# Optimization experiments

Hardware: AMD Instinct MI355X
Metric: run time of the kernel (lower is better)

Reference implementation:

```python
import jax, jax.numpy as jnp
import numpy as np

WS = 4        # window size
NH = 8        # num heads
GN_GROUPS = 8 # min(8, hidden_dim)
EPS = 1e-5


def group_norm(x, gamma, beta, groups=GN_GROUPS, eps=EPS):
    # x: [B, C, H, W]
    B, C, H, W = x.shape
    xr = x.reshape(B, groups, C // groups, H, W)
    mu = xr.mean(axis=(2, 3, 4), keepdims=True)
    var = xr.var(axis=(2, 3, 4), keepdims=True)
    xn = ((xr - mu) / jnp.sqrt(var + eps)).reshape(B, C, H, W)
    return xn * gamma[None, :, None, None] + beta[None, :, None, None]


def setup_inputs() -> dict:
    key = jax.random.key(0)
    ks = jax.random.split(key, 8)
    B, Cin, Ch, H, W = 4, 64, 256, 128, 128
    sc = 0.02
    return {
        "x": jax.random.normal(ks[0], (B, Cin, H, W), dtype=jnp.float32),
        "h": jax.random.normal(ks[1], (B, Ch, H, W), dtype=jnp.float32),
        "c": jax.random.normal(ks[2], (B, Ch, H, W), dtype=jnp.float32),
        "in_proj_w": jax.random.normal(ks[3], (Ch, Cin + Ch), dtype=jnp.float32) * sc,
        "in_proj_b": jnp.zeros((Ch,), jnp.float32),
        "ln_g": jnp.ones((Ch,), jnp.float32),
        "ln_b": jnp.zeros((Ch,), jnp.float32),
        "qkv_w": jax.random.normal(ks[4], (3 * Ch, Ch), dtype=jnp.float32) * sc,
        "qkv_b": jnp.zeros((3 * Ch,), jnp.float32),
        "proj_w": jax.random.normal(ks[5], (Ch, Ch), dtype=jnp.float32) * sc,
        "proj_b": jnp.zeros((Ch,), jnp.float32),
        "gates_w": jax.random.normal(ks[6], (4 * Ch, Ch), dtype=jnp.float32) * sc,
        "gates_b": jnp.zeros((4 * Ch,), jnp.float32),
        "gn_g": jnp.ones((Ch,), jnp.float32),
        "gn_b": jnp.zeros((Ch,), jnp.float32),
    }


def reference(x, h, c, in_proj_w, in_proj_b, ln_g, ln_b, qkv_w, qkv_b,
              proj_w, proj_b, gates_w, gates_b, gn_g, gn_b):
    B, Cin, H, W = x.shape
    Ch = h.shape[1]
    ws, nh = WS, NH
    hd = Ch // nh
    nHw, nWw = H // ws, W // ws  # H,W divisible by ws -> no padding branch

    # in_proj: 1x1 conv on concat([x, h])
    comb = jnp.concatenate([x, h], axis=1)  # [B, Cin+Ch, H, W]
    p = jnp.einsum('bchw,oc->bohw', comb, in_proj_w) + in_proj_b[None, :, None, None]

    # window partition -> [B*nWin, ws*ws, Ch]
    xw = p.reshape(B, Ch, nHw, ws, nWw, ws)
    xw = xw.transpose(0, 2, 4, 3, 5, 1).reshape(B * nHw * nWw, ws * ws, Ch)

    # pre-attention LayerNorm
    mu = xw.mean(-1, keepdims=True)
    var = xw.var(-1, keepdims=True)
    xn = (xw - mu) / jnp.sqrt(var + EPS) * ln_g + ln_b

    # multi-head attention within each 16-token window
    Bw, N, _ = xn.shape
    qkv = (xn @ qkv_w.T + qkv_b).reshape(Bw, N, 3, nh, hd)
    q, k, v = qkv[:, :, 0], qkv[:, :, 1], qkv[:, :, 2]  # [Bw, N, nh, hd]
    attn = jnp.einsum('bqhd,bkhd->bhqk', q, k) * (hd ** -0.5)
    attn = jax.nn.softmax(attn, axis=-1)
    out = jnp.einsum('bhqk,bkhd->bqhd', attn, v).reshape(Bw, N, Ch)
    out = out @ proj_w.T + proj_b

    # window unpartition -> [B, Ch, H, W]
    am = out.reshape(B, nHw, nWw, ws, ws, Ch)
    am = am.transpose(0, 5, 1, 3, 2, 4).reshape(B, Ch, H, W)

    am = group_norm(am, gn_g, gn_b)  # eval mode: dropout2d is identity

    # LSTM gates via 1x1 conv
    gates = jnp.einsum('bchw,oc->bohw', am, gates_w) + gates_b[None, :, None, None]
    ci, cf, co, cg = jnp.split(gates, 4, axis=1)
    i = jax.nn.sigmoid(ci)
    f = jax.nn.sigmoid(cf)
    o = jax.nn.sigmoid(co)
    g = jnp.tanh(cg)
    cnext = f * c + i * g
    hnext = group_norm(o * jnp.tanh(cnext), gn_g, gn_b)
    return hnext, cnext
```

## Files before the change

### kernel.cpp

```cpp
#include <hip/hip_runtime.h>

#define DI __device__ __forceinline__

typedef unsigned short ushort_t;
typedef __attribute__((ext_vector_type(8))) short bf16x8;
typedef __attribute__((ext_vector_type(4))) float f32x4;
typedef __attribute__((ext_vector_type(4))) unsigned short us4;
typedef __attribute__((ext_vector_type(8))) unsigned short us8;

constexpr float EPSF = 1e-5f;

constexpr size_t O_WIP  = 0;
constexpr size_t O_WQKV = 163840;
constexpr size_t O_WPRJ = 557056;
constexpr size_t O_WGAT = 688128;
constexpr size_t O_MU   = 1212416;
constexpr size_t O_RSTD = 1474560;
constexpr size_t O_GN   = 1736704;
constexpr size_t O_FIN  = 1737216;
constexpr size_t O_R2   = 1740800;
constexpr size_t O_R3   = O_R2 + 33554432;
constexpr size_t O_R1   = O_R3 + 33554432;

DI ushort_t f2b(float f) {
  unsigned u = __float_as_uint(f);
  u += 0x7fff + ((u >> 16) & 1);
  return (ushort_t)(u >> 16);
}
DI float b2f(ushort_t s) { return __uint_as_float(((unsigned)s) << 16); }

DI void cp16(ushort_t* lds, const ushort_t* g) {
  __builtin_amdgcn_global_load_lds(
      (const __attribute__((address_space(1))) unsigned*)g,
      (__attribute__((address_space(3))) unsigned*)lds, 16, 0, 0);
}

__global__ __launch_bounds__(256) void k_prep(const float* __restrict__ ipw,
    const float* __restrict__ qkvw, const float* __restrict__ projw,
    const float* __restrict__ gatesw, ushort_t* __restrict__ d0,
    ushort_t* __restrict__ d1, ushort_t* __restrict__ d2, ushort_t* __restrict__ d3) {
  int i = blockIdx.x * 256 + threadIdx.x;
  if (i < 81920)  { d0[i] = f2b(ipw[i]);    return; }
  i -= 81920;
  if (i < 196608) { d1[i] = f2b(qkvw[i]);   return; }
  i -= 196608;
  if (i < 65536)  { d2[i] = f2b(projw[i]);  return; }
  i -= 65536;
  if (i < 262144) { d3[i] = f2b(gatesw[i]); return; }
}

__global__ __launch_bounds__(256) void k_comb(const float* __restrict__ x,
    const float* __restrict__ h, ushort_t* __restrict__ comb) {
  __shared__ float tile[32][257];
  const int tid = threadIdx.x;
  const int wid = blockIdx.x;
  const int b = wid / 640, r = wid % 640, ct = r / 64, pt = r % 64;
  const int p0 = pt * 256;
#pragma unroll 8
  for (int i = 0; i < 32; ++i) {
    const int cg = ct * 32 + i;
    const float* src = (cg < 64) ? x + (((size_t)(b * 64 + cg)) << 14)
                                 : h + (((size_t)(b * 256 + (cg - 64))) << 14);
    tile[i][tid] = src[p0 + tid];
  }
  __syncthreads();
  const int c = tid & 31;
#pragma unroll 8
  for (int i2 = 0; i2 < 32; ++i2) {
    const int tl = (tid >> 5) + i2 * 8;
    comb[(size_t)((b << 14) + p0 + tl) * 320 + ct * 32 + c] = f2b(tile[c][tl]);
  }
}

template<int K, int KT, bool GATESB>
DI void gemm_main(const ushort_t* __restrict__ A, const ushort_t* __restrict__ B,
                  int t0, int nb, ushort_t* smem, f32x4 acc[4][4]) {
  const int tid = threadIdx.x;
  const int lane = tid & 63, wave = tid >> 6;
  const int w2 = wave * 2;
  const int wm = wave >> 1, wn = wave & 1;
  const int kfs = lane >> 4, cc = lane & 15;
  const int aoff = kfs * 1024 + (wm * 64 + cc) * 8;
  const int boff = 4096 + kfs * 1024 + (wn * 64 + cc) * 8;

  auto stage = [&](int buf, int k0) {
#pragma unroll
    for (int i = 0; i < 2; ++i) {
      const int w2i = w2 + i;
      const int kslot = w2i >> 1;
      const int mrow = ((w2i & 1) << 6) + lane;
      const ushort_t* ga = A + (size_t)(t0 + mrow) * K + k0 + kslot * 8;
      cp16(smem + buf * 8192 + w2i * 512, ga);
      int ng;
      if (GATESB) ng = ((mrow >> 5) << 8) + nb + (mrow & 31);
      else        ng = nb + mrow;
      const ushort_t* gb = B + (size_t)ng * K + k0 + kslot * 8;
      cp16(smem + buf * 8192 + 4096 + w2i * 512, gb);
    }
  };

  stage(0, 0);
  __syncthreads();
  for (int kt = 0; kt < KT; ++kt) {
    const int cur = (kt & 1) * 8192;
    if (kt + 1 < KT) stage((kt & 1) ^ 1, (kt + 1) * 32);
    bf16x8 a0 = *(const bf16x8*)(smem + cur + aoff);
    bf16x8 a1 = *(const bf16x8*)(smem + cur + aoff + 128);
    bf16x8 a2 = *(const bf16x8*)(smem + cur + aoff + 256);
    bf16x8 a3 = *(const bf16x8*)(smem + cur + aoff + 384);
    bf16x8 b0 = *(const bf16x8*)(smem + cur + boff);
    bf16x8 b1 = *(const bf16x8*)(smem + cur + boff + 128);
    bf16x8 b2 = *(const bf16x8*)(smem + cur + boff + 256);
    bf16x8 b3 = *(const bf16x8*)(smem + cur + boff + 384);
    acc[0][0] = __builtin_amdgcn_mfma_f32_16x16x32_bf16(a0, b0, acc[0][0], 0, 0, 0);
    acc[0][1] = __builtin_amdgcn_mfma_f32_16x16x32_bf16(a0, b1, acc[0][1], 0, 0, 0);
    acc[0][2] = __builtin_amdgcn_mfma_f32_16x16x32_bf16(a0, b2, acc[0][2], 0, 0, 0);
    acc[0][3] = __builtin_amdgcn_mfma_f32_16x16x32_bf16(a0, b3, acc[0][3], 0, 0, 0);
    acc[1][0] = __builtin_amdgcn_mfma_f32_16x16x32_bf16(a1, b0, acc[1][0], 0, 0, 0);
    acc[1][1] = __builtin_amdgcn_mfma_f32_16x16x32_bf16(a1, b1, acc[1][1], 0, 0, 0);
    acc[1][2] = __builtin_amdgcn_mfma_f32_16x16x32_bf16(a1, b2, acc[1][2], 0, 0, 0);
    acc[1][3] = __builtin_amdgcn_mfma_f32_16x16x32_bf16(a1, b3, acc[1][3], 0, 0, 0);
    acc[2][0] = __builtin_amdgcn_mfma_f32_16x16x32_bf16(a2, b0, acc[2][0], 0, 0, 0);
    acc[2][1] = __builtin_amdgcn_mfma_f32_16x16x32_bf16(a2, b1, acc[2][1], 0, 0, 0);
    acc[2][2] = __builtin_amdgcn_mfma_f32_16x16x32_bf16(a2, b2, acc[2][2], 0, 0, 0);
    acc[2][3] = __builtin_amdgcn_mfma_f32_16x16x32_bf16(a2, b3, acc[2][3], 0, 0, 0);
    acc[3][0] = __builtin_amdgcn_mfma_f32_16x16x32_bf16(a3, b0, acc[3][0], 0, 0, 0);
    acc[3][1] = __builtin_amdgcn_mfma_f32_16x16x32_bf16(a3, b1, acc[3][1], 0, 0, 0);
    acc[3][2] = __builtin_amdgcn_mfma_f32_16x16x32_bf16(a3, b2, acc[3][2], 0, 0, 0);
    acc[3][3] = __builtin_amdgcn_mfma_f32_16x16x32_bf16(a3, b3, acc[3][3], 0, 0, 0);
    __syncthreads();
  }
}

template<int NTOT>
DI void epi_store(f32x4 acc[4][4], ushort_t* __restrict__ C, const float* __restrict__ bias,
                  int t0, int n0g) {
  const int tid = threadIdx.x, lane = tid & 63, wave = tid >> 6;
  const int wm = wave >> 1, wn = wave & 1;
  const int r0 = (lane >> 4) * 4, cc = lane & 15;
#pragma unroll
  for (int fn = 0; fn < 4; ++fn) {
    const int n = wn * 64 + fn * 16 + cc;
    const float bv = bias[n0g + n];
#pragma unroll
    for (int fm = 0; fm < 4; ++fm) {
#pragma unroll
      for (int r = 0; r < 4; ++r) {
        const int m = wm * 64 + fm * 16 + r0 + r;
        C[(size_t)(t0 + m) * NTOT + n0g + n] = f2b(acc[fm][fn][r] + bv);
      }
    }
  }
}

__global__ __launch_bounds__(256) void k_inproj(const ushort_t* __restrict__ A,
    const ushort_t* __restrict__ B, const float* __restrict__ bias, ushort_t* __restrict__ C) {
  __shared__ ushort_t smem[16384];
  const int wid = blockIdx.x, g = wid & 7, s = wid >> 3;
  const int mt = g * 64 + s / 2, nt = s % 2;
  f32x4 acc[4][4] = {};
  gemm_main<320, 10, false>(A, B, mt * 128, nt * 128, smem, acc);
  epi_store<256>(acc, C, bias, mt * 128, nt * 128);
}

__global__ __launch_bounds__(256) void k_qkv(const ushort_t* __restrict__ A,
    const ushort_t* __restrict__ B, const float* __restrict__ bias, ushort_t* __restrict__ C) {
  __shared__ ushort_t smem[16384];
  const int wid = blockIdx.x, g = wid & 7, s = wid >> 3;
  const int mt = g * 64 + s / 6, nt = s % 6;
  f32x4 acc[4][4] = {};
  gemm_main<256, 8, false>(A, B, mt * 128, nt * 128, smem, acc);
  epi_store<768>(acc, C, bias, mt * 128, nt * 128);
}

__global__ __launch_bounds__(256) void k_proj(const ushort_t* __restrict__ A,
    const ushort_t* __restrict__ B, const float* __restrict__ bias, ushort_t* __restrict__ C,
    float* __restrict__ gnsum) {
  __shared__ ushort_t smem[16384];
  const int wid = blockIdx.x, g = wid & 7, s = wid >> 3;
  const int mt = g * 64 + s / 2, nt = s % 2;
  const int t0 = mt * 128, n0g = nt * 128;
  f32x4 acc[4][4] = {};
  gemm_main<256, 8, false>(A, B, t0, n0g, smem, acc);
  const int tid = threadIdx.x, lane = tid & 63, wave = tid >> 6;
  const int wm = wave >> 1, wn = wave & 1;
  const int r0 = (lane >> 4) * 4, cc = lane & 15;
  float sA = 0.f, s2A = 0.f, sB = 0.f, s2B = 0.f;
#pragma unroll
  for (int fn = 0; fn < 4; ++fn) {
    const int n = wn * 64 + fn * 16 + cc;
    const float bv = bias[n0g + n];
#pragma unroll
    for (int fm = 0; fm < 4; ++fm) {
#pragma unroll
      for (int r = 0; r < 4; ++r) {
        const int m = wm * 64 + fm * 16 + r0 + r;
        const float v = acc[fm][fn][r] + bv;
        C[(size_t)(t0 + m) * 256 + n0g + n] = f2b(v);
        if (fn < 2) { sA += v; s2A += v * v; } else { sB += v; s2B += v * v; }
      }
    }
  }
#pragma unroll
  for (int o = 32; o; o >>= 1) {
    sA += __shfl_down(sA, o); s2A += __shfl_down(s2A, o);
    sB += __shfl_down(sB, o); s2B += __shfl_down(s2B, o);
  }
  if (lane == 0) {
    const int bch = t0 >> 14;
    const int gb0 = (n0g >> 5) + wn * 2;
    atomicAdd(&gnsum[bch * 8 + gb0], sA);      atomicAdd(&gnsum[32 + bch * 8 + gb0], s2A);
    atomicAdd(&gnsum[bch * 8 + gb0 + 1], sB);  atomicAdd(&gnsum[32 + bch * 8 + gb0 + 1], s2B);
  }
}

__global__ __launch_bounds__(256) void k_gates(const ushort_t* __restrict__ A,
    const ushort_t* __restrict__ B, const float* __restrict__ gbias,
    const float* __restrict__ cin, float* __restrict__ cnext, float* __restrict__ u,
    float* __restrict__ gnsum2) {
  __shared__ ushort_t smem[16512];
  const int wid = blockIdx.x, g = wid & 7, s = wid >> 3;
  const int mt = g * 64 + (s >> 3), nt = s & 7;
  const int t0 = mt * 128, ch0 = nt * 32;
  f32x4 acc[4][4] = {};
  gemm_main<256, 8, true>(A, B, t0, ch0, smem, acc);

  float* cs = (float*)smem;
  const int tid = threadIdx.x, lane = tid & 63, wave = tid >> 6;
  const int wm = wave >> 1, wn = wave & 1;
  const int r0 = (lane >> 4) * 4, cc = lane & 15;
  const int bch = t0 >> 14, pix0 = t0 & 16383;
  const int cl = tid >> 3, tq = tid & 7;
  const int ch = ch0 + cl;
  const float bi = gbias[ch], bf_ = gbias[256 + ch];
  const float bo = gbias[512 + ch], bg = gbias[768 + ch];
  float ssum = 0.f, ssq = 0.f;
#pragma unroll
  for (int mh = 0; mh < 2; ++mh) {
    __syncthreads();
    if (wm == mh) {
#pragma unroll
      for (int fm = 0; fm < 4; ++fm)
#pragma unroll
        for (int fn = 0; fn < 4; ++fn)
#pragma unroll
          for (int r = 0; r < 4; ++r)
            cs[(fm * 16 + r0 + r) * 129 + wn * 64 + fn * 16 + cc] = acc[fm][fn][r];
    }
    __syncthreads();
    const size_t base = (((size_t)(bch * 256 + ch)) << 14) + pix0 + mh * 64 + tq * 8;
    float cv[8], cn[8], uv[8];
    *(float4*)cv       = *(const float4*)(cin + base);
    *(float4*)(cv + 4) = *(const float4*)(cin + base + 4);
#pragma unroll
    for (int i = 0; i < 8; ++i) {
      const int t = tq * 8 + i;
      const float zi = cs[t * 129 + cl] + bi;
      const float zf = cs[t * 129 + 32 + cl] + bf_;
      const float zo = cs[t * 129 + 64 + cl] + bo;
      const float zg = cs[t * 129 + 96 + cl] + bg;
      const float iv = 1.f / (1.f + expf(-zi));
      const float fv = 1.f / (1.f + expf(-zf));
      const float ov = 1.f / (1.f + expf(-zo));
      const float gv = tanhf(zg);
      const float c2 = fv * cv[i] + iv * gv;
      cn[i] = c2;
      const float uu = ov * tanhf(c2);
      uv[i] = uu; ssum += uu; ssq += uu * uu;
    }
    *(float4*)(cnext + base)     = *(float4*)cn;
    *(float4*)(cnext + base + 4) = *(float4*)(cn + 4);
    *(float4*)(u + base)         = *(float4*)uv;
    *(float4*)(u + base + 4)     = *(float4*)(uv + 4);
  }
#pragma unroll
  for (int o = 32; o; o >>= 1) { ssum += __shfl_down(ssum, o); ssq += __shfl_down(ssq, o); }
  if (lane == 0) {
    atomicAdd(&gnsum2[bch * 8 + nt], ssum);
    atomicAdd(&gnsum2[32 + bch * 8 + nt], ssq);
  }
}

__global__ __launch_bounds__(256) void k_lnstats(const ushort_t* __restrict__ p,
    float* __restrict__ mu, float* __restrict__ rstd) {
  const int wave = threadIdx.x >> 6, lane = threadIdx.x & 63;
  const int t = blockIdx.x * 4 + wave;
  us4 v = *(const us4*)(p + (size_t)t * 256 + lane * 4);
  const float a = b2f(v[0]), b = b2f(v[1]), c = b2f(v[2]), d = b2f(v[3]);
  float s = a + b + c + d, s2 = a * a + b * b + c * c + d * d;
#pragma unroll
  for (int o = 32; o; o >>= 1) { s += __shfl_down(s, o); s2 += __shfl_down(s2, o); }
  if (lane == 0) {
    const float m = s * (1.f / 256.f);
    const float var = s2 * (1.f / 256.f) - m * m;
    mu[t] = m;
    rstd[t] = rsqrtf(fmaxf(var, 0.f) + EPSF);
  }
}

__global__ __launch_bounds__(256) void k_xn(const ushort_t* __restrict__ p,
    const float* __restrict__ mu, const float* __restrict__ rstd,
    const float* __restrict__ lg, const float* __restrict__ lb, ushort_t* __restrict__ xn) {
  const size_t i = ((size_t)blockIdx.x * 256 + threadIdx.x) * 8;
  const int t = (int)(i >> 8), c = (int)(i & 255);
  const float m = mu[t], r = rstd[t];
  us8 v = *(const us8*)(p + i);
  us8 o;
#pragma unroll
  for (int e = 0; e < 8; ++e)
    o[e] = f2b((b2f(v[e]) - m) * r * lg[c + e] + lb[c + e]);
  *(us8*)(xn + i) = o;
}

__global__ __launch_bounds__(128) void k_attn(const ushort_t* __restrict__ qkvb,
    ushort_t* __restrict__ ao) {
  __shared__ float ks[4224], vs[4224];
  const int tid = threadIdx.x;
  const int wid = blockIdx.x;
  const int b = wid >> 10, rem = wid & 1023, wh = rem >> 5, wc = rem & 31;
  const int tbase = (b << 14) + wh * 512 + wc * 4;
#pragma unroll 4
  for (int it = 0; it < 16; ++it) {
    const int i = it * 128 + tid;
    const int j = i >> 7, q = i & 127;
    const int which = q >> 6, hh2 = (q >> 3) & 7, d4 = (q & 7) << 2;
    const int tj = tbase + ((j >> 2) << 7) + (j & 3);
    us4 v = *(const us4*)(qkvb + (size_t)tj * 768 + 256 + which * 256 + hh2 * 32 + d4);
    float* dst = (which ? vs : ks) + (hh2 * 16 + j) * 33 + d4;
    dst[0] = b2f(v[0]); dst[1] = b2f(v[1]); dst[2] = b2f(v[2]); dst[3] = b2f(v[3]);
  }
  const int hh = tid >> 4, qi = tid & 15;
  const int tq = tbase + ((qi >> 2) << 7) + (qi & 3);
  float qv[32];
  {
    const ushort_t* qp = qkvb + (size_t)tq * 768 + hh * 32;
#pragma unroll
    for (int uq = 0; uq < 8; ++uq) {
      us4 v = *(const us4*)(qp + uq * 4);
#pragma unroll
      for (int e = 0; e < 4; ++e) qv[uq * 4 + e] = b2f(v[e]);
    }
  }
  __syncthreads();
  float sc[16];
#pragma unroll
  for (int j = 0; j < 16; ++j) {
    const float* kr = ks + (hh * 16 + j) * 33;
    float s = 0.f;
#pragma unroll
    for (int u2 = 0; u2 < 32; ++u2) s = fmaf(qv[u2], kr[u2], s);
    sc[j] = s * 0.17677669529663687f;
  }
  float m = sc[0];
#pragma unroll
  for (int j = 1; j < 16; ++j) m = fmaxf(m, sc[j]);
  float ssum = 0.f;
#pragma unroll
  for (int j = 0; j < 16; ++j) { sc[j] = __expf(sc[j] - m); ssum += sc[j]; }
  const float inv = 1.f / ssum;
  float oacc[32] = {};
#pragma unroll
  for (int j = 0; j < 16; ++j) {
    const float p = sc[j] * inv;
    const float* vr = vs + (hh * 16 + j) * 33;
#pragma unroll
    for (int u2 = 0; u2 < 32; ++u2) oacc[u2] = fmaf(p, vr[u2], oacc[u2]);
  }
  unsigned* dst = (unsigned*)(ao + (size_t)tq * 256 + hh * 32);
#pragma unroll
  for (int uq = 0; uq < 16; ++uq)
    dst[uq] = (unsigned)f2b(oacc[2 * uq]) | ((unsigned)f2b(oacc[2 * uq + 1]) << 16);
}

__global__ void k_gnfin(const float* __restrict__ sums, float* __restrict__ fin) {
  const int i = threadIdx.x;
  const float invN = 1.f / 524288.f;
  const float m = sums[i] * invN;
  const float var = sums[32 + i] * invN - m * m;
  fin[i] = m;
  fin[32 + i] = rsqrtf(fmaxf(var, 0.f) + EPSF);
}

__global__ __launch_bounds__(256) void k_amn(const ushort_t* __restrict__ am,
    const float* __restrict__ fin, const float* __restrict__ gg,
    const float* __restrict__ gb, ushort_t* __restrict__ amn) {
  const size_t i = ((size_t)blockIdx.x * 256 + threadIdx.x) * 8;
  const int t = (int)(i >> 8), c = (int)(i & 255);
  const int b = t >> 14, grp = c >> 5;
  const float m = fin[b * 8 + grp], r = fin[32 + b * 8 + grp];
  us8 v = *(const us8*)(am + i);
  us8 o;
#pragma unroll
  for (int e = 0; e < 8; ++e)
    o[e] = f2b((b2f(v[e]) - m) * r * gg[c + e] + gb[c + e]);
  *(us8*)(amn + i) = o;
}

__global__ __launch_bounds__(256) void k_gnapply(const float* __restrict__ u,
    const float* __restrict__ fin2, const float* __restrict__ gg,
    const float* __restrict__ gb, float* __restrict__ hout) {
  const size_t base = ((size_t)blockIdx.x * 256 + threadIdx.x) * 4;
  const int b = (int)(base >> 22);
  const int ch = (int)((base >> 14) & 255);
  const int grp = ch >> 5;
  const float m = fin2[b * 8 + grp], r = fin2[32 + b * 8 + grp];
  const float gv = gg[ch], bv = gb[ch];
  float4 v = *(const float4*)(u + base);
  v.x = (v.x - m) * r * gv + bv;
  v.y = (v.y - m) * r * gv + bv;
  v.z = (v.z - m) * r * gv + bv;
  v.w = (v.w - m) * r * gv + bv;
  *(float4*)(hout + base) = v;
}

extern "C" void kernel_launch(void* const* d_in, const int* in_sizes, int n_in,
                              void* d_out, int out_size, void* d_ws, size_t ws_size,
                              hipStream_t stream) {
  const float* x      = (const float*)d_in[0];
  const float* h      = (const float*)d_in[1];
  const float* c      = (const float*)d_in[2];
  const float* ipw    = (const float*)d_in[3];
  const float* ipb    = (const float*)d_in[4];
  const float* lng    = (const float*)d_in[5];
  const float* lnb    = (const float*)d_in[6];
  const float* qkvw   = (const float*)d_in[7];
  const float* qkvb   = (const float*)d_in[8];
  const float* projw  = (const float*)d_in[9];
  const float* projb  = (const float*)d_in[10];
  const float* gatesw = (const float*)d_in[11];
  const float* gatesb = (const float*)d_in[12];
  const float* gng    = (const float*)d_in[13];
  const float* gnb    = (const float*)d_in[14];
  char* wsb  = (char*)d_ws;
  float* out = (float*)d_out;

  ushort_t* wip  = (ushort_t*)(wsb + O_WIP);
  ushort_t* wqkv = (ushort_t*)(wsb + O_WQKV);
  ushort_t* wprj = (ushort_t*)(wsb + O_WPRJ);
  ushort_t* wgat = (ushort_t*)(wsb + O_WGAT);
  float* mu_a    = (float*)(wsb + O_MU);
  float* rstd_a  = (float*)(wsb + O_RSTD);
  float* gnsum   = (float*)(wsb + O_GN);
  float* gnfin   = (float*)(wsb + O_FIN);
  ushort_t* R2   = (ushort_t*)(wsb + O_R2);
  ushort_t* R3   = (ushort_t*)(wsb + O_R3);
  ushort_t* R1   = (ushort_t*)(wsb + O_R1);

  hipMemsetAsync(gnsum, 0, 512, stream);
  k_prep<<<2368, 256, 0, stream>>>(ipw, qkvw, projw, gatesw, wip, wqkv, wprj, wgat);
  k_comb<<<2560, 256, 0, stream>>>(x, h, R1);
  k_inproj<<<1024, 256, 0, stream>>>(R1, wip, ipb, R2);
  k_lnstats<<<16384, 256, 0, stream>>>(R2, mu_a, rstd_a);
  k_xn<<<8192, 256, 0, stream>>>(R2, mu_a, rstd_a, lng, lnb, R3);
  k_qkv<<<3072, 256, 0, stream>>>(R3, wqkv, qkvb, R1);
  k_attn<<<4096, 128, 0, stream>>>(R1, R2);
  k_proj<<<1024, 256, 0, stream>>>(R2, wprj, projb, R3, gnsum);
  k_gnfin<<<1, 32, 0, stream>>>(gnsum, gnfin);
  k_amn<<<8192, 256, 0, stream>>>(R3, gnfin, gng, gnb, R2);
  k_gates<<<4096, 256, 0, stream>>>(R2, wgat, gatesb, c, out + 16777216, (float*)R1,
                                    gnsum + 64);
  k_gnfin<<<1, 32, 0, stream>>>(gnsum + 64, gnfin + 64);
  k_gnapply<<<16384, 256, 0, stream>>>((float*)R1, gnfin + 64, gng, gnb, out);
}
```

Before: 821.1 us.

## Fuse LayerNorm into in_proj GEMM and compute LSTM gates in registers

Replaces the in_proj GEMM plus separate LN-stats and normalize kernels with one kernel that uses 64-token by 256-channel tiles, so each block holds full rows and can compute LayerNorm in its epilogue. This drops two launches and one round trip of the bf16 intermediate through global memory. The gates kernel reorders which weight rows it loads, so each wave's accumulators hold the i/f/o/g gates for the same channels. The epilogue therefore works straight from registers with no LDS transpose and no syncs, using fast exp-based sigmoid/tanh at some accuracy cost. The new in_proj tile has less per-block reuse of A, and the gates kernel now does 4-wide stores instead of 8-wide.

```diff
diff --git a/kernel.cpp b/kernel.cpp
--- a/kernel.cpp
+++ b/kernel.cpp
@@ -14,8 +14,6 @@
 constexpr size_t O_WQKV = 163840;
 constexpr size_t O_WPRJ = 557056;
 constexpr size_t O_WGAT = 688128;
-constexpr size_t O_MU   = 1212416;
-constexpr size_t O_RSTD = 1474560;
 constexpr size_t O_GN   = 1736704;
 constexpr size_t O_FIN  = 1737216;
 constexpr size_t O_R2   = 1740800;
@@ -28,6 +26,13 @@
   return (ushort_t)(u >> 16);
 }
 DI float b2f(ushort_t s) { return __uint_as_float(((unsigned)s) << 16); }
+
+DI float fsig(float x) { return 1.f / (1.f + __expf(-x)); }
+DI float ftanh(float x) {
+  const float e = __expf(-2.f * fabsf(x));
+  const float t = (1.f - e) / (1.f + e);
+  return copysignf(t, x);
+}
 
 DI void cp16(ushort_t* lds, const ushort_t* g) {
   __builtin_amdgcn_global_load_lds(
@@ -92,7 +97,7 @@
       const ushort_t* ga = A + (size_t)(t0 + mrow) * K + k0 + kslot * 8;
       cp16(smem + buf * 8192 + w2i * 512, ga);
       int ng;
-      if (GATESB) ng = ((mrow >> 5) << 8) + nb + (mrow & 31);
+      if (GATESB) ng = ((mrow >> 4) & 3) * 256 + nb + ((mrow >> 6) << 4) + (mrow & 15);
       else        ng = nb + mrow;
       const ushort_t* gb = B + (size_t)ng * K + k0 + kslot * 8;
       cp16(smem + buf * 8192 + 4096 + w2i * 512, gb);
@@ -153,14 +158,97 @@
   }
 }
 
-__global__ __launch_bounds__(256) void k_inproj(const ushort_t* __restrict__ A,
-    const ushort_t* __restrict__ B, const float* __restrict__ bias, ushort_t* __restrict__ C) {
-  __shared__ ushort_t smem[16384];
-  const int wid = blockIdx.x, g = wid & 7, s = wid >> 3;
-  const int mt = g * 64 + s / 2, nt = s % 2;
+__global__ __launch_bounds__(256) void k_inproj_ln(const ushort_t* __restrict__ A,
+    const ushort_t* __restrict__ B, const float* __restrict__ bias,
+    const float* __restrict__ lg, const float* __restrict__ lb, ushort_t* __restrict__ xn) {
+  __shared__ ushort_t smem[20480];
+  __shared__ float red[4][2][64];
+  __shared__ float fin[2][64];
+  const int tid = threadIdx.x, lane = tid & 63, wave = tid >> 6;
+  const int t0 = blockIdx.x * 64;
+  const int kfs = lane >> 4, cc = lane & 15;
+  const int r0 = kfs * 4;
+  const int aoff = kfs * 512 + cc * 8;
+  const int boff = 2048 + kfs * 2048 + (wave * 64 + cc) * 8;
+
+  auto stage = [&](int buf, int k0) {
+#pragma unroll
+    for (int rr = 0; rr < 5; ++rr) {
+      const int r = wave * 5 + rr;
+      const int e = r * 64 + lane;
+      const ushort_t* src;
+      if (r < 4) src = A + (size_t)(t0 + (e & 63)) * 320 + k0 + (e >> 6) * 8;
+      else { const int e2 = e - 256; src = B + (size_t)(e2 & 255) * 320 + k0 + (e2 >> 8) * 8; }
+      cp16(smem + buf * 10240 + r * 512, src);
+    }
+  };
+
+  stage(0, 0);
   f32x4 acc[4][4] = {};
-  gemm_main<320, 10, false>(A, B, mt * 128, nt * 128, smem, acc);
-  epi_store<256>(acc, C, bias, mt * 128, nt * 128);
+  __syncthreads();
+  for (int kt = 0; kt < 10; ++kt) {
+    const int cur = (kt & 1) * 10240;
+    if (kt < 9) stage((kt & 1) ^ 1, (kt + 1) * 32);
+    bf16x8 av[4], bv[4];
+#pragma unroll
+    for (int i = 0; i < 4; ++i) av[i] = *(const bf16x8*)(smem + cur + aoff + i * 128);
+#pragma unroll
+    for (int j = 0; j < 4; ++j) bv[j] = *(const bf16x8*)(smem + cur + boff + j * 128);
+#pragma unroll
+    for (int i = 0; i < 4; ++i)
+#pragma unroll
+      for (int j = 0; j < 4; ++j)
+        acc[i][j] = __builtin_amdgcn_mfma_f32_16x16x32_bf16(av[i], bv[j], acc[i][j], 0, 0, 0);
+    __syncthreads();
+  }
+  float bcol[4];
+#pragma unroll
+  for (int j = 0; j < 4; ++j) bcol[j] = bias[wave * 64 + j * 16 + cc];
+#pragma unroll
+  for (int i = 0; i < 4; ++i)
+#pragma unroll
+    for (int j = 0; j < 4; ++j)
+#pragma unroll
+      for (int r = 0; r < 4; ++r) acc[i][j][r] += bcol[j];
+#pragma unroll
+  for (int i = 0; i < 4; ++i) {
+#pragma unroll
+    for (int r = 0; r < 4; ++r) {
+      float s  = acc[i][0][r] + acc[i][1][r] + acc[i][2][r] + acc[i][3][r];
+      float s2 = acc[i][0][r] * acc[i][0][r] + acc[i][1][r] * acc[i][1][r]
+               + acc[i][2][r] * acc[i][2][r] + acc[i][3][r] * acc[i][3][r];
+#pragma unroll
+      for (int m = 1; m < 16; m <<= 1) { s += __shfl_xor(s, m); s2 += __shfl_xor(s2, m); }
+      if (cc == 0) { red[wave][0][i * 16 + r0 + r] = s; red[wave][1][i * 16 + r0 + r] = s2; }
+    }
+  }
+  __syncthreads();
+  if (tid < 64) {
+    const float s  = red[0][0][tid] + red[1][0][tid] + red[2][0][tid] + red[3][0][tid];
+    const float s2 = red[0][1][tid] + red[1][1][tid] + red[2][1][tid] + red[3][1][tid];
+    const float m = s * (1.f / 256.f);
+    const float var = s2 * (1.f / 256.f) - m * m;
+    fin[0][tid] = m;
+    fin[1][tid] = rsqrtf(fmaxf(var, 0.f) + EPSF);
+  }
+  __syncthreads();
+  float lgv[4], lbv[4];
+#pragma unroll
+  for (int j = 0; j < 4; ++j) {
+    const int n = wave * 64 + j * 16 + cc;
+    lgv[j] = lg[n]; lbv[j] = lb[n];
+  }
+#pragma unroll
+  for (int i = 0; i < 4; ++i)
+#pragma unroll
+    for (int r = 0; r < 4; ++r) {
+      const int m = i * 16 + r0 + r;
+      const float mu = fin[0][m], rs = fin[1][m];
+      ushort_t* dst = xn + (size_t)(t0 + m) * 256 + wave * 64 + cc;
+#pragma unroll
+      for (int j = 0; j < 4; ++j)
+        dst[j * 16] = f2b((acc[i][j][r] - mu) * rs * lgv[j] + lbv[j]);
+    }
 }
 
 __global__ __launch_bounds__(256) void k_qkv(const ushort_t* __restrict__ A,
@@ -218,60 +306,41 @@
     const ushort_t* __restrict__ B, const float* __restrict__ gbias,
     const float* __restrict__ cin, float* __restrict__ cnext, float* __restrict__ u,
     float* __restrict__ gnsum2) {
-  __shared__ ushort_t smem[16512];
+  __shared__ ushort_t smem[16384];
   const int wid = blockIdx.x, g = wid & 7, s = wid >> 3;
   const int mt = g * 64 + (s >> 3), nt = s & 7;
   const int t0 = mt * 128, ch0 = nt * 32;
   f32x4 acc[4][4] = {};
   gemm_main<256, 8, true>(A, B, t0, ch0, smem, acc);
 
-  float* cs = (float*)smem;
   const int tid = threadIdx.x, lane = tid & 63, wave = tid >> 6;
   const int wm = wave >> 1, wn = wave & 1;
   const int r0 = (lane >> 4) * 4, cc = lane & 15;
   const int bch = t0 >> 14, pix0 = t0 & 16383;
-  const int cl = tid >> 3, tq = tid & 7;
-  const int ch = ch0 + cl;
+  const int ch = ch0 + wn * 16 + cc;
   const float bi = gbias[ch], bf_ = gbias[256 + ch];
   const float bo = gbias[512 + ch], bg = gbias[768 + ch];
+  const size_t chbase = ((size_t)(bch * 256 + ch)) << 14;
   float ssum = 0.f, ssq = 0.f;
 #pragma unroll
-  for (int mh = 0; mh < 2; ++mh) {
-    __syncthreads();
-    if (wm == mh) {
-#pragma unroll
-      for (int fm = 0; fm < 4; ++fm)
-#pragma unroll
-        for (int fn = 0; fn < 4; ++fn)
-#pragma unroll
-          for (int r = 0; r < 4; ++r)
-            cs[(fm * 16 + r0 + r) * 129 + wn * 64 + fn * 16 + cc] = acc[fm][fn][r];
-    }
-    __syncthreads();
-    const size_t base = (((size_t)(bch * 256 + ch)) << 14) + pix0 + mh * 64 + tq * 8;
-    float cv[8], cn[8], uv[8];
-    *(float4*)cv       = *(const float4*)(cin + base);
-    *(float4*)(cv + 4) = *(const float4*)(cin + base + 4);
-#pragma unroll
-    for (int i = 0; i < 8; ++i) {
-      const int t = tq * 8 + i;
-      const float zi = cs[t * 129 + cl] + bi;
-      const float zf = cs[t * 129 + 32 + cl] + bf_;
-      const float zo = cs[t * 129 + 64 + cl] + bo;
-      const float zg = cs[t * 129 + 96 + cl] + bg;
-      const float iv = 1.f / (1.f + expf(-zi));
-      const float fv = 1.f / (1.f + expf(-zf));
-      const float ov = 1.f / (1.f + expf(-zo));
-      const float gv = tanhf(zg);
-      const float c2 = fv * cv[i] + iv * gv;
-      cn[i] = c2;
-      const float uu = ov * tanhf(c2);
-      uv[i] = uu; ssum += uu; ssq += uu * uu;
-    }
-    *(float4*)(cnext + base)     = *(float4*)cn;
-    *(float4*)(cnext + base + 4) = *(float4*)(cn + 4);
-    *(float4*)(u + base)         = *(float4*)uv;
-    *(float4*)(u + base + 4)     = *(float4*)(uv + 4);
+  for (int fm = 0; fm < 4; ++fm) {
+    const int pix = pix0 + wm * 64 + fm * 16 + r0;
+    const float4 cv = *(const float4*)(cin + chbase + pix);
+    float cn[4], uv[4];
+#pragma unroll
+    for (int r = 0; r < 4; ++r) {
+      const float iv = fsig(acc[fm][0][r] + bi);
+      const float fv = fsig(acc[fm][1][r] + bf_);
+      const float ov = fsig(acc[fm][2][r] + bo);
+      const float gv = ftanh(acc[fm][3][r] + bg);
+      const float cold = (&cv.x)[r];
+      const float c2 = fv * cold + iv * gv;
+      cn[r] = c2;
+      const float uu = ov * ftanh(c2);
+      uv[r] = uu; ssum += uu; ssq += uu * uu;
+    }
+    *(float4*)(cnext + chbase + pix) = *(float4*)cn;
+    *(float4*)(u + chbase + pix)     = *(float4*)uv;
   }
 #pragma unroll
   for (int o = 32; o; o >>= 1) { ssum += __shfl_down(ssum, o); ssq += __shfl_down(ssq, o); }
@@ -279,37 +348,6 @@
     atomicAdd(&gnsum2[bch * 8 + nt], ssum);
     atomicAdd(&gnsum2[32 + bch * 8 + nt], ssq);
   }
-}
-
-__global__ __launch_bounds__(256) void k_lnstats(const ushort_t* __restrict__ p,
-    float* __restrict__ mu, float* __restrict__ rstd) {
-  const int wave = threadIdx.x >> 6, lane = threadIdx.x & 63;
-  const int t = blockIdx.x * 4 + wave;
-  us4 v = *(const us4*)(p + (size_t)t * 256 + lane * 4);
-  const float a = b2f(v[0]), b = b2f(v[1]), c = b2f(v[2]), d = b2f(v[3]);
-  float s = a + b + c + d, s2 = a * a + b * b + c * c + d * d;
-#pragma unroll
-  for (int o = 32; o; o >>= 1) { s += __shfl_down(s, o); s2 += __shfl_down(s2, o); }
-  if (lane == 0) {
-    const float m = s * (1.f / 256.f);
-    const float var = s2 * (1.f / 256.f) - m * m;
-    mu[t] = m;
-    rstd[t] = rsqrtf(fmaxf(var, 0.f) + EPSF);
-  }
-}
-
-__global__ __launch_bounds__(256) void k_xn(const ushort_t* __restrict__ p,
-    const float* __restrict__ mu, const float* __restrict__ rstd,
-    const float* __restrict__ lg, const float* __restrict__ lb, ushort_t* __restrict__ xn) {
-  const size_t i = ((size_t)blockIdx.x * 256 + threadIdx.x) * 8;
-  const int t = (int)(i >> 8), c = (int)(i & 255);
-  const float m = mu[t], r = rstd[t];
-  us8 v = *(const us8*)(p + i);
-  us8 o;
-#pragma unroll
-  for (int e = 0; e < 8; ++e)
-    o[e] = f2b((b2f(v[e]) - m) * r * lg[c + e] + lb[c + e]);
-  *(us8*)(xn + i) = o;
 }
 
 __global__ __launch_bounds__(128) void k_attn(const ushort_t* __restrict__ qkvb,
@@ -438,8 +476,6 @@
   ushort_t* wqkv = (ushort_t*)(wsb + O_WQKV);
   ushort_t* wprj = (ushort_t*)(wsb + O_WPRJ);
   ushort_t* wgat = (ushort_t*)(wsb + O_WGAT);
-  float* mu_a    = (float*)(wsb + O_MU);
-  float* rstd_a  = (float*)(wsb + O_RSTD);
   float* gnsum   = (float*)(wsb + O_GN);
   float* gnfin   = (float*)(wsb + O_FIN);
   ushort_t* R2   = (ushort_t*)(wsb + O_R2);
@@ -449,9 +485,7 @@
   hipMemsetAsync(gnsum, 0, 512, stream);
   k_prep<<<2368, 256, 0, stream>>>(ipw, qkvw, projw, gatesw, wip, wqkv, wprj, wgat);
   k_comb<<<2560, 256, 0, stream>>>(x, h, R1);
-  k_inproj<<<1024, 256, 0, stream>>>(R1, wip, ipb, R2);
-  k_lnstats<<<16384, 256, 0, stream>>>(R2, mu_a, rstd_a);
-  k_xn<<<8192, 256, 0, stream>>>(R2, mu_a, rstd_a, lng, lnb, R3);
+  k_inproj_ln<<<1024, 256, 0, stream>>>(R1, wip, ipb, lng, lnb, R3);
   k_qkv<<<3072, 256, 0, stream>>>(R3, wqkv, qkvb, R1);
   k_attn<<<4096, 128, 0, stream>>>(R1, R2);
   k_proj<<<1024, 256, 0, stream>>>(R2, wprj, projb, R3, gnsum);
```

After: 789.5 us. 3.8% less time.
